# Performance work log

Measured on AMD Instinct MI355X. Metric: run time of the kernel, lower is better.

## Reference

```python
import jax, jax.numpy as jnp
import numpy as np

WS = 7           # window size
N = WS * WS      # tokens per window = 49
C = 128          # embed dim
H = 4            # heads
HD = C // H      # head dim = 32
NW = 64          # num windows (mask leading dim)
B = 4096         # total windows = outer_batch * NW


def _relative_indexes():
    ch = np.arange(WS)
    cw = np.arange(WS)
    coords = np.stack(np.meshgrid(ch, cw, indexing='ij')).reshape(2, -1)  # [2, N]
    rel = coords[:, :, None] - coords[:, None, :]                          # [2, N, N]
    rel = rel.transpose(1, 2, 0)
    rel[:, :, 0] += WS - 1
    rel[:, :, 1] += WS - 1
    rel[:, :, 0] *= 2 * WS - 1
    return jnp.asarray(rel.sum(-1), dtype=jnp.int32)                       # [N, N]


def setup_inputs() -> dict:
    key = jax.random.key(0)
    ks = jax.random.split(key, 10)
    s = 0.02
    return {
        'query': jax.random.normal(ks[0], (B, N, C), jnp.float32),
        'source': jax.random.normal(ks[1], (B, N, C), jnp.float32),
        'mask': jnp.zeros((NW, N, N), jnp.float32),
        'q_w': jax.random.normal(ks[2], (C, C), jnp.float32) * s,
        'q_b': jnp.zeros((C,), jnp.float32),
        'kv_w': jax.random.normal(ks[3], (C, 2 * C), jnp.float32) * s,
        'kv_b': jnp.zeros((2 * C,), jnp.float32),
        'proj_w': jax.random.normal(ks[4], (C, C), jnp.float32) * s,
        'proj_b': jnp.zeros((C,), jnp.float32),
        'bias_table': jax.random.normal(ks[5], ((2 * WS - 1) ** 2, H), jnp.float32) * s,
        'rel_idx': _relative_indexes(),
    }


def reference(query, source, mask, q_w, q_b, kv_w, kv_b, proj_w, proj_b, bias_table, rel_idx):
    scale = HD ** -0.5
    q = query @ q_w + q_b                       # [B, N, C]
    kv = source @ kv_w + kv_b                   # [B, N, 2C]
    k, v = kv[..., :C], kv[..., C:]
    # [B, N, H, HD] -> [B, H, N, HD]
    q = q.reshape(B, N, H, HD).transpose(0, 2, 1, 3) * scale
    k = k.reshape(B, N, H, HD).transpose(0, 2, 1, 3)
    v = v.reshape(B, N, H, HD).transpose(0, 2, 1, 3)
    attn = jnp.einsum('bhnd,bhmd->bhnm', q, k)  # [B, H, N, N]
    # gathered relative positional bias: [1, H, N, N]
    bias = bias_table[rel_idx.reshape(-1)].reshape(N, N, H).transpose(2, 0, 1)[None]
    attn = attn + bias
    # mask: [NW, N, N] broadcast over outer batch and heads
    attn = attn.reshape(-1, NW, H, N, N) + mask[None, :, None]
    attn = attn.reshape(B, H, N, N)
    attn = jax.nn.softmax(attn, axis=-1)
    x = jnp.einsum('bhnm,bhmd->bnhd', attn, v).reshape(B, N, C)
    return x @ proj_w + proj_b
```

## Files before the change

### kernel.cpp

```cpp
#include <hip/hip_runtime.h>
#include <hip/hip_bf16.h>

#define NN 49
#define CC 128
#define HH 4
#define NWIN 64
#define BB 4096
#define QSCALE 0.17677669529663687f

typedef __attribute__((ext_vector_type(8))) short bf16x8;
typedef __attribute__((ext_vector_type(4))) float f32x4;
typedef unsigned short u16;
typedef unsigned int u32;

__device__ __forceinline__ u16 f2b(float f) {
    __hip_bfloat16 h = __float2bfloat16(f);
    return __builtin_bit_cast(u16, h);
}
__device__ __forceinline__ float b2f(u16 u) { return __uint_as_float(((u32)u) << 16); }
__device__ __forceinline__ uint2 pack4(float a, float b, float c, float d) {
    uint2 r;
    r.x = (u32)f2b(a) | ((u32)f2b(b) << 16);
    r.y = (u32)f2b(c) | ((u32)f2b(d) << 16);
    return r;
}
__device__ __forceinline__ f32x4 mfma16(bf16x8 a, bf16x8 b, f32x4 c) {
    return __builtin_amdgcn_mfma_f32_16x16x32_bf16(a, b, c, 0, 0, 0);
}
__device__ __forceinline__ char* adr256(u16* base, int row, int byte) {
    return (char*)base + row * 256 + (byte ^ ((row & 7) << 4));
}
__device__ __forceinline__ char* adr128(u16* base, int row, int byte) {
    return (char*)base + row * 128 + (byte ^ ((row & 7) << 4));
}

__global__ void prep_cbt(const float* __restrict__ bias_table, const int* __restrict__ rel_idx,
                         const float* __restrict__ mask, u16* __restrict__ cbt) {
    int idx = blockIdx.x * blockDim.x + threadIdx.x;
    int m = idx & 63, i = (idx >> 6) & 63, h = (idx >> 12) & 3, wv = idx >> 14;
    if (wv >= NWIN) return;
    float v = -1e9f;
    if (m < NN && i < NN)
        v = bias_table[rel_idx[i * NN + m] * HH + h] + mask[(wv * NN + i) * NN + m];
    cbt[idx] = f2b(v);
}

__global__ void prep_w(const float* __restrict__ qw, const float* __restrict__ qb,
                       const float* __restrict__ kvw, const float* __restrict__ pjw,
                       u16* __restrict__ qwp, u16* __restrict__ kvwp,
                       u16* __restrict__ pjwp, float* __restrict__ qbs) {
    int idx = blockIdx.x * blockDim.x + threadIdx.x;
    if (idx < 16384) {
        int i = idx & 7, lane = (idx >> 3) & 63, kt = (idx >> 9) & 3, nt = idx >> 11;
        int k = 32 * kt + 8 * (lane >> 4) + i, n = 16 * nt + (lane & 15);
        qwp[idx] = f2b(qw[k * CC + n] * QSCALE);
    } else if (idx < 49152) {
        int j = idx - 16384;
        int i = j & 7, lane = (j >> 3) & 63, kt = (j >> 9) & 3, nt = j >> 11;
        int k = 32 * kt + 8 * (lane >> 4) + i, n = 16 * nt + (lane & 15);
        kvwp[j] = f2b(kvw[k * 2 * CC + n]);
    } else if (idx < 65536) {
        int j = idx - 49152;
        int i = j & 7, lane = (j >> 3) & 63, kt = (j >> 9) & 3, nt = j >> 11;
        int k = 32 * kt + 8 * (lane >> 4) + i, n = 16 * nt + (lane & 15);
        pjwp[j] = f2b(pjw[k * CC + n]);
    } else if (idx < 65664) {
        int j = idx - 65536;
        qbs[j] = qb[j] * QSCALE;
    }
}

__global__ __launch_bounds__(512, 2)
void wmha_main(const float* __restrict__ query, const float* __restrict__ source,
               const u16* __restrict__ qwp, const u16* __restrict__ kvwp,
               const u16* __restrict__ pjwp, const float* __restrict__ qbs,
               const float* __restrict__ kv_b, const float* __restrict__ proj_b,
               const u16* __restrict__ cbt, float* __restrict__ out) {
    __shared__ u16 lds[40960];
    u16* SQ = lds;
    u16* SS = lds + 8192;
    u16* Qb = lds + 16384;
    u16* Kb = lds + 24576;
    u16* VT = lds + 32768;
    const int t = threadIdx.x;
    const int b = blockIdx.x;
    const int w = t >> 6, lane = t & 63;
    const int lq = lane & 15, qd = lane >> 4;
    const int mw = w >> 2;
    const int nw = w & 3;
    const int h = w >> 1;
    const int half = w & 1;

    {
        const int row = t >> 3, qu = t & 7;
        const size_t gbase = (size_t)b * NN * CC + row * CC + qu * 8;
        #pragma unroll
        for (int j = 0; j < 2; ++j) {
            bf16x8 vq = {0,0,0,0,0,0,0,0}, vs = {0,0,0,0,0,0,0,0};
            if (row < NN) {
                const float4* q4 = (const float4*)(query + gbase) + 16 * j;
                const float4* s4 = (const float4*)(source + gbase) + 16 * j;
                float4 a0 = q4[0], a1 = q4[1], c0 = s4[0], c1 = s4[1];
                vq[0]=(short)f2b(a0.x); vq[1]=(short)f2b(a0.y); vq[2]=(short)f2b(a0.z); vq[3]=(short)f2b(a0.w);
                vq[4]=(short)f2b(a1.x); vq[5]=(short)f2b(a1.y); vq[6]=(short)f2b(a1.z); vq[7]=(short)f2b(a1.w);
                vs[0]=(short)f2b(c0.x); vs[1]=(short)f2b(c0.y); vs[2]=(short)f2b(c0.z); vs[3]=(short)f2b(c0.w);
                vs[4]=(short)f2b(c1.x); vs[5]=(short)f2b(c1.y); vs[6]=(short)f2b(c1.z); vs[7]=(short)f2b(c1.w);
            }
            *(bf16x8*)adr256(SQ, row, qu * 16 + 128 * j) = vq;
            *(bf16x8*)adr256(SS, row, qu * 16 + 128 * j) = vs;
        }
    }
    bf16x8 bwq[2][4];
    #pragma unroll
    for (int n2 = 0; n2 < 2; ++n2)
        #pragma unroll
        for (int kt = 0; kt < 4; ++kt)
            bwq[n2][kt] = *(const bf16x8*)(qwp + (((nw + 4 * n2) * 4 + kt) * 64 + lane) * 8);
    __syncthreads();

    {
        f32x4 acc[2][2] = {};
        #pragma unroll
        for (int m2 = 0; m2 < 2; ++m2) {
            bf16x8 a[4];
            #pragma unroll
            for (int kt = 0; kt < 4; ++kt)
                a[kt] = *(const bf16x8*)adr256(SQ, (2 * mw + m2) * 16 + lq, kt * 64 + qd * 16);
            __builtin_amdgcn_s_setprio(1);
            #pragma unroll
            for (int n2 = 0; n2 < 2; ++n2)
                #pragma unroll
                for (int kt = 0; kt < 4; ++kt)
                    acc[m2][n2] = mfma16(bwq[n2][kt], a[kt], acc[m2][n2]);
            __builtin_amdgcn_s_setprio(0);
        }
        #pragma unroll
        for (int n2 = 0; n2 < 2; ++n2) {
            const int cb0 = 16 * (nw + 4 * n2) + 4 * qd;
            const float4 bia = *(const float4*)(qbs + cb0);
            #pragma unroll
            for (int m2 = 0; m2 < 2; ++m2) {
                const int tok = (2 * mw + m2) * 16 + lq;
                uint2 pk = pack4(acc[m2][n2][0] + bia.x, acc[m2][n2][1] + bia.y,
                                 acc[m2][n2][2] + bia.z, acc[m2][n2][3] + bia.w);
                *(uint2*)adr256(Qb, tok, 2 * cb0) = pk;
            }
        }
    }
    {
        bf16x8 as[2][4];
        #pragma unroll
        for (int m2 = 0; m2 < 2; ++m2)
            #pragma unroll
            for (int kt = 0; kt < 4; ++kt)
                as[m2][kt] = *(const bf16x8*)adr256(SS, (2 * mw + m2) * 16 + lq, kt * 64 + qd * 16);
        {
            bf16x8 bwk[2][4];
            #pragma unroll
            for (int n2 = 0; n2 < 2; ++n2)
                #pragma unroll
                for (int kt = 0; kt < 4; ++kt)
                    bwk[n2][kt] = *(const bf16x8*)(kvwp + (((nw + 4 * n2) * 4 + kt) * 64 + lane) * 8);
            f32x4 acc[2][2] = {};
            __builtin_amdgcn_s_setprio(1);
            #pragma unroll
            for (int m2 = 0; m2 < 2; ++m2)
                #pragma unroll
                for (int n2 = 0; n2 < 2; ++n2)
                    #pragma unroll
                    for (int kt = 0; kt < 4; ++kt)
                        acc[m2][n2] = mfma16(bwk[n2][kt], as[m2][kt], acc[m2][n2]);
            __builtin_amdgcn_s_setprio(0);
            #pragma unroll
            for (int n2 = 0; n2 < 2; ++n2) {
                const int cb0 = 16 * (nw + 4 * n2) + 4 * qd;
                const float4 bia = *(const float4*)(kv_b + cb0);
                #pragma unroll
                for (int m2 = 0; m2 < 2; ++m2) {
                    const int tok = (2 * mw + m2) * 16 + lq;
                    uint2 pk = pack4(acc[m2][n2][0] + bia.x, acc[m2][n2][1] + bia.y,
                                     acc[m2][n2][2] + bia.z, acc[m2][n2][3] + bia.w);
                    *(uint2*)adr256(Kb, tok, 2 * cb0) = pk;
                }
            }
        }
        {
            bf16x8 bwv[2][4];
            #pragma unroll
            for (int n2 = 0; n2 < 2; ++n2)
                #pragma unroll
                for (int kt = 0; kt < 4; ++kt)
                    bwv[n2][kt] = *(const bf16x8*)(kvwp + (((8 + nw + 4 * n2) * 4 + kt) * 64 + lane) * 8);
            f32x4 acc[2][2] = {};
            __builtin_amdgcn_s_setprio(1);
            #pragma unroll
            for (int m2 = 0; m2 < 2; ++m2)
                #pragma unroll
                for (int n2 = 0; n2 < 2; ++n2)
                    #pragma unroll
                    for (int kt = 0; kt < 4; ++kt)
                        acc[m2][n2] = mfma16(as[m2][kt], bwv[n2][kt], acc[m2][n2]);
            __builtin_amdgcn_s_setprio(0);
            #pragma unroll
            for (int n2 = 0; n2 < 2; ++n2) {
                const int dim = 16 * (nw + 4 * n2) + lq;
                const float bias = kv_b[CC + dim];
                #pragma unroll
                for (int m2 = 0; m2 < 2; ++m2) {
                    uint2 pk = pack4(acc[m2][n2][0] + bias, acc[m2][n2][1] + bias,
                                     acc[m2][n2][2] + bias, acc[m2][n2][3] + bias);
                    *(uint2*)adr128(VT, dim, 2 * ((2 * mw + m2) * 16 + qd * 4)) = pk;
                }
            }
        }
    }
    __syncthreads();

    f32x4 s[2][4];
    {
        bf16x8 kf[4], qf[2];
        #pragma unroll
        for (int a = 0; a < 4; ++a)
            kf[a] = *(const bf16x8*)adr256(Kb, a * 16 + lq, h * 64 + qd * 16);
        #pragma unroll
        for (int i = 0; i < 2; ++i)
            qf[i] = *(const bf16x8*)adr256(Qb, (2 * half + i) * 16 + lq, h * 64 + qd * 16);
        __builtin_amdgcn_s_setprio(1);
        #pragma unroll
        for (int i = 0; i < 2; ++i) {
            f32x4 z = {0.f, 0.f, 0.f, 0.f};
            #pragma unroll
            for (int a = 0; a < 4; ++a)
                s[i][a] = mfma16(kf[a], qf[i], z);
        }
        __builtin_amdgcn_s_setprio(0);
    }
    {
        bf16x8 vf[2][2];
        #pragma unroll
        for (int dt = 0; dt < 2; ++dt)
            #pragma unroll
            for (int kt = 0; kt < 2; ++kt)
                vf[dt][kt] = *(const bf16x8*)adr128(VT, h * 32 + dt * 16 + lq, kt * 64 + qd * 16);
        u16* pb = SS + w * 1024;
        const u16* cbb = cbt + ((size_t)((b & (NWIN - 1)) * HH + h) << 12);
        #pragma unroll
        for (int i = 0; i < 2; ++i) {
            const int bq = 2 * half + i;
            uint2 cb2[4];
            #pragma unroll
            for (int a = 0; a < 4; ++a)
                cb2[a] = *(const uint2*)(cbb + (bq * 16 + lq) * 64 + a * 16 + qd * 4);
            #pragma unroll
            for (int a = 0; a < 4; ++a) {
                s[i][a][0] += b2f((u16)(cb2[a].x & 0xffffu));
                s[i][a][1] += b2f((u16)(cb2[a].x >> 16));
                s[i][a][2] += b2f((u16)(cb2[a].y & 0xffffu));
                s[i][a][3] += b2f((u16)(cb2[a].y >> 16));
            }
            float m0 = s[i][0][0];
            #pragma unroll
            for (int a = 0; a < 4; ++a)
                #pragma unroll
                for (int r = 0; r < 4; ++r) m0 = fmaxf(m0, s[i][a][r]);
            m0 = fmaxf(m0, __shfl_xor(m0, 16));
            m0 = fmaxf(m0, __shfl_xor(m0, 32));
            uint2 pk[4];
            float sm = 0.f;
            #pragma unroll
            for (int a = 0; a < 4; ++a) {
                float p0 = __expf(s[i][a][0] - m0), p1 = __expf(s[i][a][1] - m0);
                float p2 = __expf(s[i][a][2] - m0), p3 = __expf(s[i][a][3] - m0);
                pk[a] = pack4(p0, p1, p2, p3);
                sm += b2f((u16)pk[a].x) + b2f((u16)(pk[a].x >> 16))
                    + b2f((u16)pk[a].y) + b2f((u16)(pk[a].y >> 16));
            }
            sm += __shfl_xor(sm, 16);
            sm += __shfl_xor(sm, 32);
            const float inv = 1.f / sm;
            #pragma unroll
            for (int a = 0; a < 4; ++a)
                *(uint2*)adr128(pb, lq, 32 * a + 8 * qd) = pk[a];
            asm volatile("s_waitcnt lgkmcnt(0)" ::: "memory");
            __builtin_amdgcn_sched_barrier(0);
            f32x4 o[2] = {{0.f,0.f,0.f,0.f},{0.f,0.f,0.f,0.f}};
            __builtin_amdgcn_s_setprio(1);
            #pragma unroll
            for (int kt = 0; kt < 2; ++kt) {
                bf16x8 pf = *(const bf16x8*)adr128(pb, lq, 64 * kt + 16 * qd);
                #pragma unroll
                for (int dt = 0; dt < 2; ++dt)
                    o[dt] = mfma16(vf[dt][kt], pf, o[dt]);
            }
            __builtin_amdgcn_s_setprio(0);
            __builtin_amdgcn_sched_barrier(0);
            #pragma unroll
            for (int dt = 0; dt < 2; ++dt) {
                uint2 px = pack4(o[dt][0] * inv, o[dt][1] * inv,
                                 o[dt][2] * inv, o[dt][3] * inv);
                *(uint2*)adr256(SQ, bq * 16 + lq, 64 * h + 32 * dt + 8 * qd) = px;
            }
        }
    }

    {
        bf16x8 bw[2][4];
        #pragma unroll
        for (int n2 = 0; n2 < 2; ++n2)
            #pragma unroll
            for (int kt = 0; kt < 4; ++kt)
                bw[n2][kt] = *(const bf16x8*)(pjwp + (((nw + 4 * n2) * 4 + kt) * 64 + lane) * 8);
        __syncthreads();
        f32x4 acc[2][2] = {};
        #pragma unroll
        for (int m2 = 0; m2 < 2; ++m2) {
            bf16x8 a[4];
            #pragma unroll
            for (int kt = 0; kt < 4; ++kt)
                a[kt] = *(const bf16x8*)adr256(SQ, (2 * mw + m2) * 16 + lq, kt * 64 + qd * 16);
            __builtin_amdgcn_s_setprio(1);
            #pragma unroll
            for (int n2 = 0; n2 < 2; ++n2)
                #pragma unroll
                for (int kt = 0; kt < 4; ++kt)
                    acc[m2][n2] = mfma16(bw[n2][kt], a[kt], acc[m2][n2]);
            __builtin_amdgcn_s_setprio(0);
        }
        float* outb = out + (size_t)b * NN * CC;
        #pragma unroll
        for (int n2 = 0; n2 < 2; ++n2) {
            const int cb0 = 16 * (nw + 4 * n2) + 4 * qd;
            const float4 bia = *(const float4*)(proj_b + cb0);
            #pragma unroll
            for (int m2 = 0; m2 < 2; ++m2) {
                const int tok = (2 * mw + m2) * 16 + lq;
                if (tok < NN) {
                    float4 vst;
                    vst.x = acc[m2][n2][0] + bia.x;
                    vst.y = acc[m2][n2][1] + bia.y;
                    vst.z = acc[m2][n2][2] + bia.z;
                    vst.w = acc[m2][n2][3] + bia.w;
                    *(float4*)(outb + tok * CC + cb0) = vst;
                }
            }
        }
    }
}

extern "C" void kernel_launch(void* const* d_in, const int* in_sizes, int n_in,
                              void* d_out, int out_size, void* d_ws, size_t ws_size,
                              hipStream_t stream) {
    const float* query      = (const float*)d_in[0];
    const float* source     = (const float*)d_in[1];
    const float* mask       = (const float*)d_in[2];
    const float* q_w        = (const float*)d_in[3];
    const float* q_b        = (const float*)d_in[4];
    const float* kv_w       = (const float*)d_in[5];
    const float* kv_b       = (const float*)d_in[6];
    const float* proj_w     = (const float*)d_in[7];
    const float* proj_b     = (const float*)d_in[8];
    const float* bias_table = (const float*)d_in[9];
    const int*   rel_idx    = (const int*)d_in[10];
    float* out = (float*)d_out;

    u16* cbt   = (u16*)d_ws;
    u16* qwp   = cbt + 1048576;
    u16* kvwp  = qwp + 16384;
    u16* pjwp  = kvwp + 32768;
    float* qbs = (float*)(pjwp + 16384);

    prep_cbt<<<4096, 256, 0, stream>>>(bias_table, rel_idx, mask, cbt);
    prep_w<<<257, 256, 0, stream>>>(q_w, q_b, kv_w, proj_w, qwp, kvwp, pjwp, qbs);
    wmha_main<<<BB, 512, 0, stream>>>(query, source, qwp, kvwp, pjwp, qbs,
                                      kv_b, proj_b, cbt, out);
}
```

Before: 125.0 us.

## Hoist weight, bias and positional-bias loads to kernel start; batch PV MFMAs

Moves the global loads for the Q/K/V weight fragments, the combined bias/mask tile and the per-column biases to the very start of the kernel, so their latency overlaps the input staging. Projection weights and biases are likewise prefetched before the QK^T stage. The softmax writes its probability tiles for both query row-blocks into the now-free Qb/Kb buffers, guarded by an extra barrier, so the two PV MFMA chains run back-to-back in a single batch. This raises register pressure considerably (about 24 extra bf16x8 weight fragments held live), which risks lower occupancy or spilling.

Result: slower. 176.5 us (+41.1%).

```diff
diff --git a/kernel.cpp b/kernel.cpp
--- a/kernel.cpp
+++ b/kernel.cpp
@@ -91,6 +91,34 @@
     const int h = w >> 1;
     const int half = w & 1;
 
+    bf16x8 bwq[2][4], bwk[2][4], bwv[2][4];
+    #pragma unroll
+    for (int n2 = 0; n2 < 2; ++n2)
+        #pragma unroll
+        for (int kt = 0; kt < 4; ++kt) {
+            bwq[n2][kt] = *(const bf16x8*)(qwp  + (((nw + 4 * n2) * 4 + kt) * 64 + lane) * 8);
+            bwk[n2][kt] = *(const bf16x8*)(kvwp + (((nw + 4 * n2) * 4 + kt) * 64 + lane) * 8);
+            bwv[n2][kt] = *(const bf16x8*)(kvwp + (((8 + nw + 4 * n2) * 4 + kt) * 64 + lane) * 8);
+        }
+    uint2 cbr[2][4];
+    {
+        const u16* cbb = cbt + ((size_t)((b & (NWIN - 1)) * HH + h) << 12);
+        #pragma unroll
+        for (int i = 0; i < 2; ++i)
+            #pragma unroll
+            for (int a = 0; a < 4; ++a)
+                cbr[i][a] = *(const uint2*)(cbb + ((2 * half + i) * 16 + lq) * 64 + a * 16 + qd * 4);
+    }
+    float4 qbia[2], kbia[2];
+    float vbia[2];
+    #pragma unroll
+    for (int n2 = 0; n2 < 2; ++n2) {
+        const int cb0 = 16 * (nw + 4 * n2) + 4 * qd;
+        qbia[n2] = *(const float4*)(qbs + cb0);
+        kbia[n2] = *(const float4*)(kv_b + cb0);
+        vbia[n2] = kv_b[CC + 16 * (nw + 4 * n2) + lq];
+    }
+
     {
         const int row = t >> 3, qu = t & 7;
         const size_t gbase = (size_t)b * NN * CC + row * CC + qu * 8;
@@ -110,12 +138,6 @@
             *(bf16x8*)adr256(SS, row, qu * 16 + 128 * j) = vs;
         }
     }
-    bf16x8 bwq[2][4];
-    #pragma unroll
-    for (int n2 = 0; n2 < 2; ++n2)
-        #pragma unroll
-        for (int kt = 0; kt < 4; ++kt)
-            bwq[n2][kt] = *(const bf16x8*)(qwp + (((nw + 4 * n2) * 4 + kt) * 64 + lane) * 8);
     __syncthreads();
 
     {
@@ -137,12 +159,11 @@
         #pragma unroll
         for (int n2 = 0; n2 < 2; ++n2) {
             const int cb0 = 16 * (nw + 4 * n2) + 4 * qd;
-            const float4 bia = *(const float4*)(qbs + cb0);
             #pragma unroll
             for (int m2 = 0; m2 < 2; ++m2) {
                 const int tok = (2 * mw + m2) * 16 + lq;
-                uint2 pk = pack4(acc[m2][n2][0] + bia.x, acc[m2][n2][1] + bia.y,
-                                 acc[m2][n2][2] + bia.z, acc[m2][n2][3] + bia.w);
+                uint2 pk = pack4(acc[m2][n2][0] + qbia[n2].x, acc[m2][n2][1] + qbia[n2].y,
+                                 acc[m2][n2][2] + qbia[n2].z, acc[m2][n2][3] + qbia[n2].w);
                 *(uint2*)adr256(Qb, tok, 2 * cb0) = pk;
             }
         }
@@ -155,12 +176,6 @@
             for (int kt = 0; kt < 4; ++kt)
                 as[m2][kt] = *(const bf16x8*)adr256(SS, (2 * mw + m2) * 16 + lq, kt * 64 + qd * 16);
         {
-            bf16x8 bwk[2][4];
-            #pragma unroll
-            for (int n2 = 0; n2 < 2; ++n2)
-                #pragma unroll
-                for (int kt = 0; kt < 4; ++kt)
-                    bwk[n2][kt] = *(const bf16x8*)(kvwp + (((nw + 4 * n2) * 4 + kt) * 64 + lane) * 8);
             f32x4 acc[2][2] = {};
             __builtin_amdgcn_s_setprio(1);
             #pragma unroll
@@ -174,23 +189,16 @@
             #pragma unroll
             for (int n2 = 0; n2 < 2; ++n2) {
                 const int cb0 = 16 * (nw + 4 * n2) + 4 * qd;
-                const float4 bia = *(const float4*)(kv_b + cb0);
                 #pragma unroll
                 for (int m2 = 0; m2 < 2; ++m2) {
                     const int tok = (2 * mw + m2) * 16 + lq;
-                    uint2 pk = pack4(acc[m2][n2][0] + bia.x, acc[m2][n2][1] + bia.y,
-                                     acc[m2][n2][2] + bia.z, acc[m2][n2][3] + bia.w);
+                    uint2 pk = pack4(acc[m2][n2][0] + kbia[n2].x, acc[m2][n2][1] + kbia[n2].y,
+                                     acc[m2][n2][2] + kbia[n2].z, acc[m2][n2][3] + kbia[n2].w);
                     *(uint2*)adr256(Kb, tok, 2 * cb0) = pk;
                 }
             }
         }
         {
-            bf16x8 bwv[2][4];
-            #pragma unroll
-            for (int n2 = 0; n2 < 2; ++n2)
-                #pragma unroll
-                for (int kt = 0; kt < 4; ++kt)
-                    bwv[n2][kt] = *(const bf16x8*)(kvwp + (((8 + nw + 4 * n2) * 4 + kt) * 64 + lane) * 8);
             f32x4 acc[2][2] = {};
             __builtin_amdgcn_s_setprio(1);
             #pragma unroll
@@ -204,7 +212,7 @@
             #pragma unroll
             for (int n2 = 0; n2 < 2; ++n2) {
                 const int dim = 16 * (nw + 4 * n2) + lq;
-                const float bias = kv_b[CC + dim];
+                const float bias = vbia[n2];
                 #pragma unroll
                 for (int m2 = 0; m2 < 2; ++m2) {
                     uint2 pk = pack4(acc[m2][n2][0] + bias, acc[m2][n2][1] + bias,
@@ -217,6 +225,16 @@
     __syncthreads();
 
     f32x4 s[2][4];
+    bf16x8 vf[2][2];
+    bf16x8 bwp[2][4];
+    float4 pbia[2];
+    #pragma unroll
+    for (int n2 = 0; n2 < 2; ++n2) {
+        #pragma unroll
+        for (int kt = 0; kt < 4; ++kt)
+            bwp[n2][kt] = *(const bf16x8*)(pjwp + (((nw + 4 * n2) * 4 + kt) * 64 + lane) * 8);
+        pbia[n2] = *(const float4*)(proj_b + 16 * (nw + 4 * n2) + 4 * qd);
+    }
     {
         bf16x8 kf[4], qf[2];
         #pragma unroll
@@ -234,29 +252,26 @@
                 s[i][a] = mfma16(kf[a], qf[i], z);
         }
         __builtin_amdgcn_s_setprio(0);
-    }
-    {
-        bf16x8 vf[2][2];
         #pragma unroll
         for (int dt = 0; dt < 2; ++dt)
             #pragma unroll
             for (int kt = 0; kt < 2; ++kt)
                 vf[dt][kt] = *(const bf16x8*)adr128(VT, h * 32 + dt * 16 + lq, kt * 64 + qd * 16);
-        u16* pb = SS + w * 1024;
-        const u16* cbb = cbt + ((size_t)((b & (NWIN - 1)) * HH + h) << 12);
+    }
+    __syncthreads();
+
+    {
+        u16* pb0 = Qb + w * 1024;
+        u16* pb1 = Kb + w * 1024;
+        float inv[2];
         #pragma unroll
         for (int i = 0; i < 2; ++i) {
-            const int bq = 2 * half + i;
-            uint2 cb2[4];
-            #pragma unroll
-            for (int a = 0; a < 4; ++a)
-                cb2[a] = *(const uint2*)(cbb + (bq * 16 + lq) * 64 + a * 16 + qd * 4);
             #pragma unroll
             for (int a = 0; a < 4; ++a) {
-                s[i][a][0] += b2f((u16)(cb2[a].x & 0xffffu));
-                s[i][a][1] += b2f((u16)(cb2[a].x >> 16));
-                s[i][a][2] += b2f((u16)(cb2[a].y & 0xffffu));
-                s[i][a][3] += b2f((u16)(cb2[a].y >> 16));
+                s[i][a][0] += b2f((u16)(cbr[i][a].x & 0xffffu));
+                s[i][a][1] += b2f((u16)(cbr[i][a].x >> 16));
+                s[i][a][2] += b2f((u16)(cbr[i][a].y & 0xffffu));
+                s[i][a][3] += b2f((u16)(cbr[i][a].y >> 16));
             }
             float m0 = s[i][0][0];
             #pragma unroll
@@ -277,40 +292,39 @@
             }
             sm += __shfl_xor(sm, 16);
             sm += __shfl_xor(sm, 32);
-            const float inv = 1.f / sm;
+            inv[i] = 1.f / sm;
+            u16* pb = i ? pb1 : pb0;
             #pragma unroll
             for (int a = 0; a < 4; ++a)
                 *(uint2*)adr128(pb, lq, 32 * a + 8 * qd) = pk[a];
-            asm volatile("s_waitcnt lgkmcnt(0)" ::: "memory");
-            __builtin_amdgcn_sched_barrier(0);
-            f32x4 o[2] = {{0.f,0.f,0.f,0.f},{0.f,0.f,0.f,0.f}};
-            __builtin_amdgcn_s_setprio(1);
-            #pragma unroll
-            for (int kt = 0; kt < 2; ++kt) {
-                bf16x8 pf = *(const bf16x8*)adr128(pb, lq, 64 * kt + 16 * qd);
-                #pragma unroll
-                for (int dt = 0; dt < 2; ++dt)
-                    o[dt] = mfma16(vf[dt][kt], pf, o[dt]);
-            }
-            __builtin_amdgcn_s_setprio(0);
-            __builtin_amdgcn_sched_barrier(0);
+        }
+        asm volatile("s_waitcnt lgkmcnt(0)" ::: "memory");
+        __builtin_amdgcn_sched_barrier(0);
+        f32x4 o[2][2] = {};
+        __builtin_amdgcn_s_setprio(1);
+        #pragma unroll
+        for (int kt = 0; kt < 2; ++kt) {
+            bf16x8 pf0 = *(const bf16x8*)adr128(pb0, lq, 64 * kt + 16 * qd);
+            bf16x8 pf1 = *(const bf16x8*)adr128(pb1, lq, 64 * kt + 16 * qd);
             #pragma unroll
             for (int dt = 0; dt < 2; ++dt) {
-                uint2 px = pack4(o[dt][0] * inv, o[dt][1] * inv,
-                                 o[dt][2] * inv, o[dt][3] * inv);
-                *(uint2*)adr256(SQ, bq * 16 + lq, 64 * h + 32 * dt + 8 * qd) = px;
-            }
-        }
-    }
-
-    {
-        bf16x8 bw[2][4];
-        #pragma unroll
-        for (int n2 = 0; n2 < 2; ++n2)
-            #pragma unroll
-            for (int kt = 0; kt < 4; ++kt)
-                bw[n2][kt] = *(const bf16x8*)(pjwp + (((nw + 4 * n2) * 4 + kt) * 64 + lane) * 8);
-        __syncthreads();
+                o[0][dt] = mfma16(vf[dt][kt], pf0, o[0][dt]);
+                o[1][dt] = mfma16(vf[dt][kt], pf1, o[1][dt]);
+            }
+        }
+        __builtin_amdgcn_s_setprio(0);
+        #pragma unroll
+        for (int i = 0; i < 2; ++i)
+            #pragma unroll
+            for (int dt = 0; dt < 2; ++dt) {
+                uint2 px = pack4(o[i][dt][0] * inv[i], o[i][dt][1] * inv[i],
+                                 o[i][dt][2] * inv[i], o[i][dt][3] * inv[i]);
+                *(uint2*)adr256(SQ, (2 * half + i) * 16 + lq, 64 * h + 32 * dt + 8 * qd) = px;
+            }
+    }
+    __syncthreads();
+
+    {
         f32x4 acc[2][2] = {};
         #pragma unroll
         for (int m2 = 0; m2 < 2; ++m2) {
@@ -323,23 +337,22 @@
             for (int n2 = 0; n2 < 2; ++n2)
                 #pragma unroll
                 for (int kt = 0; kt < 4; ++kt)
-                    acc[m2][n2] = mfma16(bw[n2][kt], a[kt], acc[m2][n2]);
+                    acc[m2][n2] = mfma16(bwp[n2][kt], a[kt], acc[m2][n2]);
             __builtin_amdgcn_s_setprio(0);
         }
         float* outb = out + (size_t)b * NN * CC;
         #pragma unroll
         for (int n2 = 0; n2 < 2; ++n2) {
             const int cb0 = 16 * (nw + 4 * n2) + 4 * qd;
-            const float4 bia = *(const float4*)(proj_b + cb0);
             #pragma unroll
             for (int m2 = 0; m2 < 2; ++m2) {
                 const int tok = (2 * mw + m2) * 16 + lq;
                 if (tok < NN) {
                     float4 vst;
-                    vst.x = acc[m2][n2][0] + bia.x;
-                    vst.y = acc[m2][n2][1] + bia.y;
-                    vst.z = acc[m2][n2][2] + bia.z;
-                    vst.w = acc[m2][n2][3] + bia.w;
+                    vst.x = acc[m2][n2][0] + pbia[n2].x;
+                    vst.y = acc[m2][n2][1] + pbia[n2].y;
+                    vst.z = acc[m2][n2][2] + pbia[n2].z;
+                    vst.w = acc[m2][n2][3] + pbia[n2].w;
                     *(float4*)(outb + tok * CC + cb0) = vst;
                 }
             }
```

## Batch both query blocks' softmax before PV MFMAs, reusing Q/K LDS for P

Applied to the files above, without the earlier changes.

The bias/mask loads for both query blocks are hoisted ahead of softmax, and V fragments are loaded early. A block-wide barrier then lets the P tiles for both blocks be written into the now-free Q and K LDS regions, so the separate SS scratch is no longer used. The PV MFMAs for both blocks are issued together after a single LDS wait instead of one wait per block. The aim is more independent MFMA and memory work per wait. The cost is an extra __syncthreads and higher register pressure from holding cbr, vf and two sets of outputs live.

After: 124.2 us. About the same (-0.7%).

```diff
diff --git a/kernel.cpp b/kernel.cpp
--- a/kernel.cpp
+++ b/kernel.cpp
@@ -217,6 +217,7 @@
     __syncthreads();
 
     f32x4 s[2][4];
+    bf16x8 vf[2][2];
     {
         bf16x8 kf[4], qf[2];
         #pragma unroll
@@ -234,29 +235,35 @@
                 s[i][a] = mfma16(kf[a], qf[i], z);
         }
         __builtin_amdgcn_s_setprio(0);
-    }
-    {
-        bf16x8 vf[2][2];
         #pragma unroll
         for (int dt = 0; dt < 2; ++dt)
             #pragma unroll
             for (int kt = 0; kt < 2; ++kt)
                 vf[dt][kt] = *(const bf16x8*)adr128(VT, h * 32 + dt * 16 + lq, kt * 64 + qd * 16);
-        u16* pb = SS + w * 1024;
+    }
+    uint2 cbr[2][4];
+    {
         const u16* cbb = cbt + ((size_t)((b & (NWIN - 1)) * HH + h) << 12);
         #pragma unroll
+        for (int i = 0; i < 2; ++i)
+            #pragma unroll
+            for (int a = 0; a < 4; ++a)
+                cbr[i][a] = *(const uint2*)(cbb + ((2 * half + i) * 16 + lq) * 64 + a * 16 + qd * 4);
+    }
+    __syncthreads();
+
+    {
+        u16* pb0 = Qb + w * 1024;
+        u16* pb1 = Kb + w * 1024;
+        float inv[2];
+        #pragma unroll
         for (int i = 0; i < 2; ++i) {
-            const int bq = 2 * half + i;
-            uint2 cb2[4];
-            #pragma unroll
-            for (int a = 0; a < 4; ++a)
-                cb2[a] = *(const uint2*)(cbb + (bq * 16 + lq) * 64 + a * 16 + qd * 4);
             #pragma unroll
             for (int a = 0; a < 4; ++a) {
-                s[i][a][0] += b2f((u16)(cb2[a].x & 0xffffu));
-                s[i][a][1] += b2f((u16)(cb2[a].x >> 16));
-                s[i][a][2] += b2f((u16)(cb2[a].y & 0xffffu));
-                s[i][a][3] += b2f((u16)(cb2[a].y >> 16));
+                s[i][a][0] += b2f((u16)(cbr[i][a].x & 0xffffu));
+                s[i][a][1] += b2f((u16)(cbr[i][a].x >> 16));
+                s[i][a][2] += b2f((u16)(cbr[i][a].y & 0xffffu));
+                s[i][a][3] += b2f((u16)(cbr[i][a].y >> 16));
             }
             float m0 = s[i][0][0];
             #pragma unroll
@@ -277,30 +284,35 @@
             }
             sm += __shfl_xor(sm, 16);
             sm += __shfl_xor(sm, 32);
-            const float inv = 1.f / sm;
+            inv[i] = 1.f / sm;
+            u16* pb = i ? pb1 : pb0;
             #pragma unroll
             for (int a = 0; a < 4; ++a)
                 *(uint2*)adr128(pb, lq, 32 * a + 8 * qd) = pk[a];
-            asm volatile("s_waitcnt lgkmcnt(0)" ::: "memory");
-            __builtin_amdgcn_sched_barrier(0);
-            f32x4 o[2] = {{0.f,0.f,0.f,0.f},{0.f,0.f,0.f,0.f}};
-            __builtin_amdgcn_s_setprio(1);
-            #pragma unroll
-            for (int kt = 0; kt < 2; ++kt) {
-                bf16x8 pf = *(const bf16x8*)adr128(pb, lq, 64 * kt + 16 * qd);
-                #pragma unroll
-                for (int dt = 0; dt < 2; ++dt)
-                    o[dt] = mfma16(vf[dt][kt], pf, o[dt]);
-            }
-            __builtin_amdgcn_s_setprio(0);
-            __builtin_amdgcn_sched_barrier(0);
+        }
+        asm volatile("s_waitcnt lgkmcnt(0)" ::: "memory");
+        __builtin_amdgcn_sched_barrier(0);
+        f32x4 o[2][2] = {};
+        __builtin_amdgcn_s_setprio(1);
+        #pragma unroll
+        for (int kt = 0; kt < 2; ++kt) {
+            bf16x8 pf0 = *(const bf16x8*)adr128(pb0, lq, 64 * kt + 16 * qd);
+            bf16x8 pf1 = *(const bf16x8*)adr128(pb1, lq, 64 * kt + 16 * qd);
             #pragma unroll
             for (int dt = 0; dt < 2; ++dt) {
-                uint2 px = pack4(o[dt][0] * inv, o[dt][1] * inv,
-                                 o[dt][2] * inv, o[dt][3] * inv);
-                *(uint2*)adr256(SQ, bq * 16 + lq, 64 * h + 32 * dt + 8 * qd) = px;
-            }
-        }
+                o[0][dt] = mfma16(vf[dt][kt], pf0, o[0][dt]);
+                o[1][dt] = mfma16(vf[dt][kt], pf1, o[1][dt]);
+            }
+        }
+        __builtin_amdgcn_s_setprio(0);
+        #pragma unroll
+        for (int i = 0; i < 2; ++i)
+            #pragma unroll
+            for (int dt = 0; dt < 2; ++dt) {
+                uint2 px = pack4(o[i][dt][0] * inv[i], o[i][dt][1] * inv[i],
+                                 o[i][dt][2] * inv[i], o[i][dt][3] * inv[i]);
+                *(uint2*)adr256(SQ, (2 * half + i) * 16 + lq, 64 * h + 32 * dt + 8 * qd) = px;
+            }
     }
 
     {
```
